# Optimization experiments

Measured on AMD Instinct MI355X. Metric: run time of the kernel, lower is better.

The kernel has to match this reference:

```python
import math
import jax, jax.numpy as jnp
import numpy as np

SCALE = 4; K = 7; R = 3; K2 = K * K
BANDS = 10; FEAT = 64; HID = 256; HEADS = 4
LH = 96; LW = 96; H = LH * SCALE; W = LW * SCALE
IN_DIM = FEAT + 4 * BANDS + 2  # 106
REF_HID = 48  # 3 groups * 16


def _conv(x, w, b, groups=1):
    y = jax.lax.conv_general_dilated(x, w, (1, 1), 'SAME',
        dimension_numbers=('NCHW', 'OIHW', 'NCHW'), feature_group_count=groups)
    return y + b[None, :, None, None]


def _gelu(x):
    return jax.nn.gelu(x, approximate=False)  # torch nn.GELU default (erf)


def _gray(x):  # [B,3,H,W] -> [B,1,H,W]
    return 0.2989 * x[:, 0:1] + 0.587 * x[:, 1:2] + 0.114 * x[:, 2:3]


def setup_inputs() -> dict:
    key = jax.random.key(0)
    ks = iter(jax.random.split(key, 64))
    def W_(sh, s=0.05):
        return (jax.random.normal(next(ks), sh, dtype=jnp.float32) * s)
    def Z_(sh):
        return jnp.zeros(sh, jnp.float32)
    d = {}
    d['lr'] = jax.random.uniform(next(ks), (1, 3, LH, LW), dtype=jnp.float32)
    d['enc_w0'] = W_((FEAT, 3, 3, 3)); d['enc_b0'] = Z_((FEAT,))
    d['enc_w1'] = W_((FEAT, FEAT, 3, 3)); d['enc_b1'] = Z_((FEAT,))
    d['enc_w2'] = W_((FEAT, FEAT, 3, 3)); d['enc_b2'] = Z_((FEAT,))
    d['enc_w3'] = W_((FEAT, FEAT, 3, 3)); d['enc_b3'] = Z_((FEAT,))
    # cond_fuser: 1x1 convs, cond_ch=2 (hover bnd+mask, zeros at inference)
    d['cond_w0'] = W_((FEAT, FEAT + 2, 1, 1)); d['cond_b0'] = Z_((FEAT,))
    d['cond_w1'] = W_((FEAT, FEAT, 1, 1)); d['cond_b1'] = Z_((FEAT,))
    # KernelMLP backbone: 5 Linear layers
    d['mlp_w0'] = W_((IN_DIM, HID)); d['mlp_b0'] = Z_((HID,))
    d['mlp_w1'] = W_((HID, HID)); d['mlp_b1'] = Z_((HID,))
    d['mlp_w2'] = W_((HID, HID)); d['mlp_b2'] = Z_((HID,))
    d['mlp_w3'] = W_((HID, HID)); d['mlp_b3'] = Z_((HID,))
    d['mlp_w4'] = W_((HID, HID)); d['mlp_b4'] = Z_((HID,))
    d['hk_w'] = W_((HID, HEADS * K2)); d['hk_b'] = Z_((HEADS * K2,))
    d['hg_w'] = W_((HID, HEADS)); d['hg_b'] = Z_((HEADS,))
    # ResidualRefiner: grouped convs, groups=3 (OIHW with in/groups channels)
    d['ref_w0'] = W_((REF_HID, 2, 3, 3)); d['ref_b0'] = Z_((REF_HID,))
    d['ref_w1'] = W_((REF_HID, 16, 3, 3)); d['ref_b1'] = Z_((REF_HID,))
    d['ref_w2'] = W_((3, 16, 3, 3)); d['ref_b2'] = Z_((3,))
    return d


def reference(lr, enc_w0, enc_b0, enc_w1, enc_b1, enc_w2, enc_b2, enc_w3, enc_b3,
              cond_w0, cond_b0, cond_w1, cond_b1,
              mlp_w0, mlp_b0, mlp_w1, mlp_b1, mlp_w2, mlp_b2, mlp_w3, mlp_b3,
              mlp_w4, mlp_b4, hk_w, hk_b, hg_w, hg_b,
              ref_w0, ref_b0, ref_w1, ref_b1, ref_w2, ref_b2):
    # --- local CNN features on LR grid ---
    f = _gelu(_conv(lr, enc_w0, enc_b0))
    f = _gelu(_conv(f, enc_w1, enc_b1))
    f = _gelu(_conv(f, enc_w2, enc_b2))
    f = _gelu(_conv(f, enc_w3, enc_b3))
    cond = jnp.zeros((1, 2, LH, LW), f.dtype)  # no hover maps at inference
    f = _conv(jnp.concatenate([f, cond], axis=1), cond_w0, cond_b0)
    f = _conv(_gelu(f), cond_w1, cond_b1)
    # --- bilinear upsample (align_corners=False semantics) ---
    lr_up = jax.image.resize(lr, (1, 3, H, W), method='bilinear')
    # --- HR pixel grid -> LR centers + fractional offsets ---
    yy, xx = jnp.meshgrid(jnp.arange(H), jnp.arange(W), indexing='ij')
    xx = xx.reshape(-1).astype(jnp.float32)
    yy = yy.reshape(-1).astype(jnp.float32)
    lx = (xx + 0.5) / SCALE - 0.5
    ly = (yy + 0.5) / SCALE - 0.5
    cx = jnp.clip(jnp.round(lx), 0, LW - 1)
    cy = jnp.clip(jnp.round(ly), 0, LH - 1)
    dx = (lx - cx)[:, None]
    dy = (ly - cy)[:, None]
    cxi = cx.astype(jnp.int32)
    cyi = cy.astype(jnp.int32)
    idx = cyi * LW + cxi  # flattened gather index [N]
    feat_flat = f[0].reshape(FEAT, -1).T  # [lh*lw, FEAT]
    cf = feat_flat[idx]                   # [N, FEAT]
    # --- Fourier PE of normalized HR coords ---
    xn = (xx + 0.5) / W * 2.0 - 1.0
    yn = (yy + 0.5) / H * 2.0 - 1.0
    freq = (2.0 ** jnp.arange(BANDS, dtype=jnp.float32)) * math.pi
    ax = xn[:, None] * freq[None, :]
    ay = yn[:, None] * freq[None, :]
    pe = jnp.stack([jnp.sin(ax), jnp.cos(ax), jnp.sin(ay), jnp.cos(ay)], axis=-1)
    pe = pe.reshape(-1, 4 * BANDS)  # per-band [sinx,cosx,siny,cosy] order
    # --- per-pixel kernel MLP ---
    z = jnp.concatenate([cf, pe, dx, dy], axis=1)  # [N, 106]
    h = _gelu(z @ mlp_w0 + mlp_b0)
    h = _gelu(h @ mlp_w1 + mlp_b1)
    h = _gelu(h @ mlp_w2 + mlp_b2)
    h = _gelu(h @ mlp_w3 + mlp_b3)
    h = _gelu(h @ mlp_w4 + mlp_b4)
    klog = (h @ hk_w + hk_b).reshape(-1, HEADS, K2)
    glog = h @ hg_w + hg_b
    ker = jax.nn.softmax(klog, axis=-1)   # non-negative kernels
    gate = jax.nn.softmax(glog, axis=-1)  # head mixture
    kmix = jnp.einsum('nh,nhk->nk', gate, ker)  # [N, K2]
    # --- gather KxK LR neighborhood and apply adaptive kernel ---
    oy, ox = jnp.meshgrid(jnp.arange(-R, R + 1), jnp.arange(-R, R + 1), indexing='ij')
    ox = ox.reshape(-1); oy = oy.reshape(-1)  # offsets: oy outer, ox inner
    nx = jnp.clip(cxi[:, None] + ox[None, :], 0, LW - 1)
    ny = jnp.clip(cyi[:, None] + oy[None, :], 0, LH - 1)
    nidx = ny * LW + nx                     # [N, K2]
    lr_flat = lr[0].reshape(3, -1).T        # [lh*lw, 3]
    patches = lr_flat[nidx]                 # [N, K2, 3]
    pred = jnp.einsum('nk,nkc->nc', kmix, patches)  # [N, 3]
    sr = pred.reshape(H, W, 3).transpose(2, 0, 1)[None]  # [1,3,H,W]
    # --- color-safe residual refiner (groups=3) ---
    res0 = sr - lr_up
    x6 = jnp.concatenate([lr_up, res0], axis=1)
    r1 = _gelu(_conv(x6, ref_w0, ref_b0, groups=3))
    r1 = _gelu(_conv(r1, ref_w1, ref_b1, groups=3))
    res = _conv(r1, ref_w2, ref_b2, groups=3)
    sr2 = sr + res
    # --- color-preserving fusion: inject only grayscale residual ---
    delta = _gray(sr2) - _gray(lr_up)
    out = jnp.clip(lr_up + delta, 0.0, 1.0)
    return out
```

## Files before the change

kernel.cpp:

```cpp
#include <hip/hip_runtime.h>
#include <math.h>

#define LWI 96
#define LHI 96
#define HWD 384
#define NPIX 147456
#define LRPIX 9216
#define HID 256

typedef __attribute__((ext_vector_type(8))) _Float16 f16x8;
typedef __attribute__((ext_vector_type(4))) _Float16 f16x4;
typedef __attribute__((ext_vector_type(16))) float f32x16;

__device__ __forceinline__ float gelu_fast(float x){
  float x2 = x*x;
  float u = x*(-2.3021181f - 0.1029443f*x2);
  float e = exp2f(u);
  return x * __builtin_amdgcn_rcpf(1.0f + e);
}

__device__ __forceinline__ float lr_up_at(const float* __restrict__ lr, int c, int y, int x){
  float sy = (y+0.5f)*0.25f - 0.5f;
  float sx = (x+0.5f)*0.25f - 0.5f;
  float fy = floorf(sy), fx = floorf(sx);
  float ty = sy - fy, tx = sx - fx;
  int y0 = (int)fy, x0 = (int)fx;
  int y0c = min(max(y0,0),LHI-1), y1c = min(max(y0+1,0),LHI-1);
  int x0c = min(max(x0,0),LWI-1), x1c = min(max(x0+1,0),LWI-1);
  const float* p = lr + c*LRPIX;
  float v00 = p[y0c*LWI+x0c], v01 = p[y0c*LWI+x1c];
  float v10 = p[y1c*LWI+x0c], v11 = p[y1c*LWI+x1c];
  return (1.f-ty)*((1.f-tx)*v00 + tx*v01) + ty*((1.f-tx)*v10 + tx*v11);
}

__global__ __launch_bounds__(256) void conv3x3_f16out(
    const float* __restrict__ in, const float* __restrict__ w,
    const float* __restrict__ b, _Float16* __restrict__ out16){
  int tid = blockIdx.x*256 + threadIdx.x;
  int o = tid / LRPIX; int rem = tid - o*LRPIX;
  int y = rem / LWI;   int x = rem - y*LWI;
  int ou = __builtin_amdgcn_readfirstlane(o);
  float acc = b[ou];
  const float* wo = w + ou*27;
  for (int i=0;i<3;++i){
    const float* inp = in + i*LRPIX;
    #pragma unroll
    for (int dy=0;dy<3;++dy){
      int yy = y + dy - 1;
      bool yok = (yy>=0 && yy<LHI);
      #pragma unroll
      for (int dx=0;dx<3;++dx){
        int xx = x + dx - 1;
        float v = (yok && xx>=0 && xx<LWI) ? inp[yy*LWI+xx] : 0.0f;
        acc = fmaf(wo[i*9 + dy*3 + dx], v, acc);
      }
    }
  }
  out16[rem*64 + o] = (_Float16)gelu_fast(acc);
}

__global__ __launch_bounds__(256) void pack_convw(
  const float* __restrict__ cw1, const float* __restrict__ cw2,
  const float* __restrict__ cw3, const float* __restrict__ xw0,
  const float* __restrict__ xw1,
  _Float16* __restrict__ WC, _Float16* __restrict__ WX)
{
  int i = blockIdx.x*256 + threadIdx.x;
  if (i < 110592){
    int cv = i / 36864; int s2 = i - cv*36864;
    int tkf = s2 >> 9; int s = s2 & 511;
    int tap = tkf >> 3; int ksfb = tkf & 7;
    int ks = ksfb >> 1; int fb = ksfb & 1;
    int slot = s >> 3; int e = s & 7;
    int oc = fb*32 + (slot & 31);
    int ic = ks*16 + (slot>>5)*8 + e;
    int dy = tap/3, dx = tap - (tap/3)*3;
    const float* src = (cv==0)?cw1:(cv==1)?cw2:cw3;
    WC[i] = (_Float16)src[((oc*64+ic)*3+dy)*3+dx];
  } else if (i < 118784){
    int j = i - 110592;
    int cv = j >> 12; int s2 = j & 4095;
    int ks = s2 >> 10; int fb = (s2 >> 9) & 1; int s = s2 & 511;
    int slot = s >> 3; int e = s & 7;
    int oc = fb*32 + (slot & 31);
    int ic = ks*16 + (slot>>5)*8 + e;
    WX[j] = (_Float16)((cv==0) ? xw0[oc*66+ic] : xw1[oc*64+ic]);
  }
}

__global__ __launch_bounds__(256) void conv_mfma_kernel(
    const _Float16* __restrict__ Xin, const _Float16* __restrict__ WC,
    const float* __restrict__ bias, _Float16* __restrict__ Xout, int cv)
{
  __shared__ _Float16 xs[100*64];
  __shared__ float red[2][2][64][20];
  const int t = threadIdx.x;
  const int lane = t & 63;
  const int w = __builtin_amdgcn_readfirstlane(t >> 6);
  const int fb = w & 1, kh = w >> 1;
  const int g = lane >> 5;
  const int gx0 = blockIdx.x*8, gy0 = blockIdx.y*8;

  for (int i = t; i < 800; i += 256){
    int sp = i >> 3, c = i & 7;
    int ly = (sp*205)>>11; int lx = sp - ly*10;
    int gy = gy0 - 1 + ly, gx = gx0 - 1 + lx;
    f16x8 v = f16x8{};
    if (gy>=0 && gy<LHI && gx>=0 && gx<LWI)
      v = *(const f16x8*)(Xin + (gy*LWI+gx)*64 + c*8);
    *(f16x8*)(xs + sp*64 + ((c ^ (sp&7))*8)) = v;
  }
  __syncthreads();

  const _Float16* WCc = WC + cv*36864;
  const int p0 = lane & 31;
  const int py0 = p0 >> 3, px0 = p0 & 7;
  f32x16 acc0{}, acc1{};
  #pragma unroll
  for (int tap = 0; tap < 9; ++tap){
    const int dy = tap/3, dx = tap - (tap/3)*3;
    #pragma unroll
    for (int ksl = 0; ksl < 2; ++ksl){
      int ks = kh*2 + ksl;
      f16x8 A = *(const f16x8*)(WCc + ((tap*4+ks)*2+fb)*512 + lane*8);
      int sp0 = (py0+dy)*10 + (px0+dx);
      int sp1 = (py0+4+dy)*10 + (px0+dx);
      int c0 = ks*2 + g;
      f16x8 B0 = *(const f16x8*)(xs + sp0*64 + ((c0 ^ (sp0&7))*8));
      f16x8 B1 = *(const f16x8*)(xs + sp1*64 + ((c0 ^ (sp1&7))*8));
      acc0 = __builtin_amdgcn_mfma_f32_32x32x16_f16(A,B0,acc0,0,0,0);
      acc1 = __builtin_amdgcn_mfma_f32_32x32x16_f16(A,B1,acc1,0,0,0);
    }
  }
  if (kh == 1){
    #pragma unroll
    for (int r4=0;r4<4;++r4){
      float4 v0 = make_float4(acc0[r4*4],acc0[r4*4+1],acc0[r4*4+2],acc0[r4*4+3]);
      float4 v1 = make_float4(acc1[r4*4],acc1[r4*4+1],acc1[r4*4+2],acc1[r4*4+3]);
      *(float4*)&red[fb][0][lane][r4*4] = v0;
      *(float4*)&red[fb][1][lane][r4*4] = v1;
    }
  }
  __syncthreads();
  if (kh == 0){
    #pragma unroll
    for (int ph=0; ph<2; ++ph){
      const f32x16& acc = ph ? acc1 : acc0;
      int py = ph*4 + py0;
      int gpx = (gy0+py)*LWI + (gx0+px0);
      #pragma unroll
      for (int r4=0;r4<4;++r4){
        float4 rr = *(const float4*)&red[fb][ph][lane][r4*4];
        float4 bb = *(const float4*)&bias[fb*32 + 8*r4 + 4*g];
        f16x4 o;
        o[0] = (_Float16)gelu_fast(acc[r4*4+0] + rr.x + bb.x);
        o[1] = (_Float16)gelu_fast(acc[r4*4+1] + rr.y + bb.y);
        o[2] = (_Float16)gelu_fast(acc[r4*4+2] + rr.z + bb.z);
        o[3] = (_Float16)gelu_fast(acc[r4*4+3] + rr.w + bb.w);
        *(f16x4*)(Xout + gpx*64 + fb*32 + 8*r4 + 4*g) = o;
      }
    }
  }
}

__global__ __launch_bounds__(256) void conv1x1_mfma(
    const _Float16* __restrict__ Xin, const _Float16* __restrict__ W1,
    const float* __restrict__ bias, _Float16* __restrict__ Xout, int dogelu)
{
  __shared__ _Float16 bufB[4096];
  const int t = threadIdx.x;
  const int lane = t & 63;
  const int w = __builtin_amdgcn_readfirstlane(t >> 6);
  const int fb = w & 1, ph = w >> 1;
  const int px0 = blockIdx.x * 64;
  #pragma unroll
  for (int h = 0; h < 2; ++h){
    int i = t + h*256;
    int p = i & 63, c = i >> 6;
    f16x8 v = *(const f16x8*)(Xin + (px0+p)*64 + c*8);
    *(f16x8*)(bufB + ((c>>1)*2 + (p>>5))*512 + ((p&31)+32*(c&1))*8) = v;
  }
  __syncthreads();
  f32x16 acc{};
  #pragma unroll
  for (int ks=0; ks<4; ++ks){
    f16x8 A = *(const f16x8*)(W1 + (ks*2+fb)*512 + lane*8);
    f16x8 B = *(const f16x8*)(bufB + (ks*2+ph)*512 + lane*8);
    acc = __builtin_amdgcn_mfma_f32_32x32x16_f16(A,B,acc,0,0,0);
  }
  const int p31 = lane & 31, hi = lane >> 5;
  int px = px0 + ph*32 + p31;
  #pragma unroll
  for (int q=0;q<4;++q){
    float4 bb = *(const float4*)&bias[fb*32 + q*8 + 4*hi];
    const float* bp = (const float*)&bb;
    f16x4 o;
    #pragma unroll
    for (int r=0;r<4;++r){
      float v = acc[q*4+r] + bp[r];
      o[r] = (_Float16)(dogelu ? gelu_fast(v) : v);
    }
    *(f16x4*)(Xout + px*64 + fb*32 + q*8 + 4*hi) = o;
  }
}

__global__ __launch_bounds__(256) void pack_weights(
  const float* __restrict__ mw0, const float* __restrict__ mw1,
  const float* __restrict__ mw2, const float* __restrict__ mw3,
  const float* __restrict__ mw4, const float* __restrict__ hkw,
  const float* __restrict__ hgw,
  const float* __restrict__ mb0, const float* __restrict__ mb1,
  const float* __restrict__ mb2, const float* __restrict__ mb3,
  const float* __restrict__ mb4, const float* __restrict__ hkb,
  const float* __restrict__ hgb,
  _Float16* __restrict__ WB, float* __restrict__ biasAll)
{
  int i = blockIdx.x*256 + threadIdx.x;
  if (i < 356352){
    int layer, local;
    if (i < 28672){ layer = 0; local = i; }
    else { layer = 1 + ((i-28672)>>16); local = (i-28672)&65535; }
    int ks = local >> 12; int r = local & 4095;
    int cb = r >> 9; int s2 = r & 511; int slot = s2 >> 3; int e = s2 & 7;
    int col = cb*32 + (slot & 31); int g = slot >> 5;
    int k = ks*16 + g*8 + e;
    float v = 0.f;
    if (layer == 0){ if (k < 106) v = mw0[k*256+col]; }
    else if (layer == 1) v = mw1[k*256+col];
    else if (layer == 2) v = mw2[k*256+col];
    else if (layer == 3) v = mw3[k*256+col];
    else if (layer == 4) v = mw4[k*256+col];
    else { if (col < 196) v = hkw[k*196+col]; else if (col < 200) v = hgw[k*4+col-196]; }
    WB[i] = (_Float16)v;
  } else if (i < 356352+1536){
    int j = i - 356352; int layer = j>>8; int col = j&255;
    float v = 0.f;
    if (layer==0) v=mb0[col]; else if (layer==1) v=mb1[col]; else if(layer==2) v=mb2[col];
    else if(layer==3) v=mb3[col]; else if(layer==4) v=mb4[col];
    else { if (col<196) v=hkb[col]; else if(col<200) v=hgb[col-196]; }
    biasAll[j] = v;
  }
}

template<int NKS>
__device__ __forceinline__ void mlp_pass(const _Float16* __restrict__ Wl,
    const _Float16* __restrict__ buf, int lane, int w, f32x16 (&acc)[2]){
  acc[0] = f32x16{}; acc[1] = f32x16{};
  #pragma unroll
  for (int ks=0; ks<NKS; ++ks){
    f16x8 a = *(const f16x8*)(Wl + (ks*8+w)*512 + lane*8);
    const _Float16* bp = buf + ks*1024 + lane*8;
    f16x8 b0 = *(const f16x8*)(bp);
    f16x8 b1 = *(const f16x8*)(bp + 512);
    acc[0] = __builtin_amdgcn_mfma_f32_32x32x16_f16(a,b0,acc[0],0,0,0);
    acc[1] = __builtin_amdgcn_mfma_f32_32x32x16_f16(a,b1,acc[1],0,0,0);
  }
}

__global__ __launch_bounds__(512,6) void mlp_mfma3_kernel(
  const _Float16* __restrict__ feat16, const float* __restrict__ lr,
  const _Float16* __restrict__ WB, const float* __restrict__ biasAll,
  float* __restrict__ sr)
{
  __shared__ _Float16 buf[16384];
  const int t = threadIdx.x;
  const int lane = t & 63;
  const int w = __builtin_amdgcn_readfirstlane(t >> 6);
  const int p31 = lane & 31; const int hi = lane >> 5;

  {
    const int p = lane; const int q = w;
    const int px = blockIdx.x*64 + p;
    const int y = px / HWD; const int x = px - y*HWD;
    float lx = (x+0.5f)*0.25f - 0.5f;
    float ly = (y+0.5f)*0.25f - 0.5f;
    float cxf = fminf(fmaxf(rintf(lx),0.f),95.f);
    float cyf = fminf(fmaxf(rintf(ly),0.f),95.f);
    int base = (int)cyf*LWI + (int)cxf;
    auto zwrite = [&](int k, float v){
      buf[((k>>4)*2 + (p>>5))*512 + ((p&31) + 32*((k>>3)&1))*8 + (k&7)] = (_Float16)v;
    };
    auto zwriteh = [&](int k, _Float16 v){
      buf[((k>>4)*2 + (p>>5))*512 + ((p&31) + 32*((k>>3)&1))*8 + (k&7)] = v;
    };
    if (q < 2){
      const _Float16* fsrc = feat16 + base*64 + q*32;
      #pragma unroll
      for (int j=0;j<32;++j) zwriteh(q*32+j, fsrc[j]);
    } else if (q == 2){
      float xn = (x+0.5f)/384.0f*2.0f - 1.0f;
      float s = sinf(xn*3.14159265358979323846f);
      float c = cosf(xn*3.14159265358979323846f);
      #pragma unroll
      for (int b=0;b<10;++b){
        zwrite(64+4*b+0, s); zwrite(64+4*b+1, c);
        float s2 = 2.f*s*c; float c2 = 1.f - 2.f*s*s;
        s=s2; c=c2;
      }
      zwrite(104, lx-cxf); zwrite(105, ly-cyf);
    } else if (q == 3){
      float yn = (y+0.5f)/384.0f*2.0f - 1.0f;
      float s = sinf(yn*3.14159265358979323846f);
      float c = cosf(yn*3.14159265358979323846f);
      #pragma unroll
      for (int b=0;b<10;++b){
        zwrite(64+4*b+2, s); zwrite(64+4*b+3, c);
        float s2 = 2.f*s*c; float c2 = 1.f - 2.f*s*s;
        s=s2; c=c2;
      }
    } else if (q == 4){
      #pragma unroll
      for (int k=106;k<112;++k) zwrite(k, 0.f);
    }
  }
  __syncthreads();

  #pragma unroll 1
  for (int L=0; L<5; ++L){
    static const int WOFFS[5] = {0,28672,94208,159744,225280};
    f32x16 acc[2];
    if (L==0) mlp_pass<7>(WB, buf, lane, w, acc);
    else      mlp_pass<16>(WB + WOFFS[L], buf, lane, w, acc);
    __syncthreads();
    const float* Bl = biasAll + L*256;
    #pragma unroll
    for (int q2=0;q2<4;++q2){
      float4 bs = *(const float4*)&Bl[w*32 + q2*8 + 4*hi];
      const float* bp2 = (const float*)&bs;
      int ks2 = w*2 + (q2>>1); int g2 = q2&1;
      _Float16* dst = buf + (ks2*2)*512 + (p31 + 32*g2)*8 + 4*hi;
      #pragma unroll
      for (int pb=0;pb<2;++pb){
        f16x4 o;
        #pragma unroll
        for (int r=0;r<4;++r) o[r] = (_Float16)gelu_fast(acc[pb][q2*4+r] + bp2[r]);
        *(f16x4*)(dst + pb*512) = o;
      }
    }
    __syncthreads();
  }

  {
    f32x16 acc[2];
    if (w < 7) mlp_pass<16>(WB + 290816, buf, lane, w, acc);
    __syncthreads();
    if (w < 7){
      #pragma unroll
      for (int reg=0;reg<16;++reg){
        int f = w*32 + (reg&3) + 8*(reg>>2) + 4*hi;
        if (f < 200){
          float bias = biasAll[1280 + f];
          buf[f*72 + p31]      = (_Float16)(acc[0][reg] + bias);
          buf[f*72 + 32 + p31] = (_Float16)(acc[1][reg] + bias);
        }
      }
    }
  }
  __syncthreads();

  if (t < 256){
    const int p = t & 63; const int hd = t >> 6;
    auto KL = [&](int col)->float { return (float)buf[col*72 + p]; };
    const float L2E = 1.4426950408889634f;
    float g0=KL(196),g1=KL(197),g2=KL(198),g3=KL(199);
    float gm = fmaxf(fmaxf(g0,g1),fmaxf(g2,g3));
    float e0=exp2f((g0-gm)*L2E),e1=exp2f((g1-gm)*L2E),
          e2=exp2f((g2-gm)*L2E),e3=exp2f((g3-gm)*L2E);
    float gate = ((hd==0)?e0:(hd==1)?e1:(hd==2)?e2:e3)/(e0+e1+e2+e3);
    float m = -1e30f;
    #pragma unroll
    for (int k=0;k<49;++k) m = fmaxf(m, KL(hd*49+k));
    float s = 0.f;
    float ev[49];
    #pragma unroll
    for (int k=0;k<49;++k){ float e=exp2f((KL(hd*49+k)-m)*L2E); s+=e; ev[k]=e; }
    float sc = gate/s;
    #pragma unroll
    for (int k=0;k<49;++k) buf[(hd*49+k)*72 + p] = (_Float16)(ev[k]*sc);
  }
  __syncthreads();

  {
    float kv[7];
    #pragma unroll
    for (int j=0;j<7;++j){
      int i = t + j*512;
      if (i < 3136){
        int k = i >> 6, p = i & 63;
        kv[j] = (float)buf[k*72+p] + (float)buf[(49+k)*72+p]
              + (float)buf[(98+k)*72+p] + (float)buf[(147+k)*72+p];
      }
    }
    __syncthreads();
    #pragma unroll
    for (int j=0;j<7;++j){
      int i = t + j*512;
      if (i < 3136){
        int k = i >> 6, p = i & 63;
        buf[k*72+p] = (_Float16)kv[j];
      }
    }
  }
  __syncthreads();

  if (t < 192){
    const int c = t >> 6; const int p = t & 63;
    const int px = blockIdx.x*64 + p;
    const int y = px / HWD; const int x = px - y*HWD;
    float lx = (x+0.5f)*0.25f - 0.5f;
    float ly = (y+0.5f)*0.25f - 0.5f;
    int cxi = (int)fminf(fmaxf(rintf(lx),0.f),95.f);
    int cyi = (int)fminf(fmaxf(rintf(ly),0.f),95.f);
    const float* lrc = lr + c*LRPIX;
    float acc = 0.f;
    bool interior = (cxi>=3 && cxi<=92 && cyi>=3 && cyi<=92);
    if (__all(interior)){
      const float* lrb = lrc + (cyi-3)*LWI + (cxi-3);
      #pragma unroll
      for (int k=0;k<49;++k){
        float km = (float)buf[k*72+p];
        acc = fmaf(km, lrb[(k/7)*LWI + (k - (k/7)*7)], acc);
      }
    } else {
      #pragma unroll
      for (int k=0;k<49;++k){
        float km = (float)buf[k*72+p];
        int oy = k/7 - 3, ox = k - (k/7)*7 - 3;
        int nyy = min(max(cyi+oy,0),95), nxx = min(max(cxi+ox,0),95);
        acc = fmaf(km, lrc[nyy*LWI+nxx], acc);
      }
    }
    sr[c*NPIX + px] = acc;
  }
}

__global__ __launch_bounds__(256) void refiner_group_kernel(
  const float* __restrict__ lr, const float* __restrict__ srg,
  const float* __restrict__ w0, const float* __restrict__ b0,
  const float* __restrict__ w1, const float* __restrict__ b1,
  const float* __restrict__ w2, const float* __restrict__ b2,
  float* __restrict__ resW)
{
  __shared__ float x6s[2][22][26];
  __shared__ float r1a[16][20][20];
  __shared__ float r1b[16][18][20];
  const int g = blockIdx.z;
  const int tid = threadIdx.x;
  const int gx0 = blockIdx.x*16, gy0 = blockIdx.y*16;

  for (int i = tid; i < 2*22*22; i += 256){
    int ic = i / 484; int rem = i - ic*484; int yy = rem / 22; int xx = rem - yy*22;
    int ch = g*2 + ic;
    int gy = gy0 - 3 + yy, gx = gx0 - 3 + xx;
    float v = 0.f;
    if (gy>=0 && gy<HWD && gx>=0 && gx<HWD){
      int c = (ch<3)?ch:(ch-3);
      float lu = lr_up_at(lr, c, gy, gx);
      v = (ch < 3) ? lu : (srg[c*NPIX + gy*HWD + gx] - lu);
    }
    x6s[ic][yy][xx] = v;
  }
  __syncthreads();

  for (int task = tid; task < 320; task += 256){
    int o = task / 20; int yy = task - o*20;
    int og = g*16 + o;
    float bias = b0[og];
    float acc[20];
    #pragma unroll
    for (int j=0;j<20;++j) acc[j] = bias;
    #pragma unroll
    for (int ic=0; ic<2; ++ic){
      #pragma unroll
      for (int dyy=0; dyy<3; ++dyy){
        float row[22];
        #pragma unroll
        for (int j=0;j<22;++j) row[j] = x6s[ic][yy+dyy][j];
        #pragma unroll
        for (int dxx=0; dxx<3; ++dxx){
          float wv = w0[((og*2+ic)*3+dyy)*3+dxx];
          #pragma unroll
          for (int j=0;j<20;++j) acc[j] = fmaf(wv, row[j+dxx], acc[j]);
        }
      }
    }
    int gyy = gy0 - 2 + yy;
    bool rok = (gyy>=0 && gyy<HWD);
    #pragma unroll
    for (int j=0;j<20;++j){
      int gxx = gx0 - 2 + j;
      r1a[o][yy][j] = (rok && gxx>=0 && gxx<HWD) ? gelu_fast(acc[j]) : 0.f;
    }
  }
  __syncthreads();

  for (int task = tid; task < 288; task += 256){
    int o = task / 18; int yy = task - o*18;
    int og = g*16 + o;
    float bias = b1[og];
    float acc[18];
    #pragma unroll
    for (int j=0;j<18;++j) acc[j] = bias;
    for (int ic=0; ic<16; ++ic){
      #pragma unroll
      for (int dyy=0; dyy<3; ++dyy){
        float row[20];
        #pragma unroll
        for (int q=0;q<5;++q)
          *(float4*)&row[q*4] = *(const float4*)&r1a[ic][yy+dyy][q*4];
        #pragma unroll
        for (int dxx=0; dxx<3; ++dxx){
          float wv = w1[((og*16+ic)*3+dyy)*3+dxx];
          #pragma unroll
          for (int j=0;j<18;++j) acc[j] = fmaf(wv, row[j+dxx], acc[j]);
        }
      }
    }
    int gyy = gy0 - 1 + yy;
    bool rok = (gyy>=0 && gyy<HWD);
    #pragma unroll
    for (int j=0;j<18;++j){
      int gxx = gx0 - 1 + j;
      r1b[o][yy][j] = (rok && gxx>=0 && gxx<HWD) ? gelu_fast(acc[j]) : 0.f;
    }
  }
  __syncthreads();

  {
    int ty = tid >> 4, tx = tid & 15;
    float a = b2[g];
    for (int ic=0; ic<16; ++ic){
      #pragma unroll
      for (int dyy=0; dyy<3; ++dyy){
        #pragma unroll
        for (int dxx=0; dxx<3; ++dxx){
          a = fmaf(w2[((g*16+ic)*3+dyy)*3+dxx], r1b[ic][ty+dyy][tx+dxx], a);
        }
      }
    }
    resW[g*NPIX + (gy0+ty)*HWD + gx0+tx] = a;
  }
}

__global__ __launch_bounds__(256) void fuse_kernel(
  const float* __restrict__ lr, const float* __restrict__ srg,
  const float* __restrict__ resW, float* __restrict__ out)
{
  int p = blockIdx.x*256 + threadIdx.x;
  int y = p / HWD, x = p - y*HWD;
  float lu[3];
  float d = 0.f;
  const float cf0=0.2989f, cf1=0.587f, cf2=0.114f;
  lu[0] = lr_up_at(lr, 0, y, x);
  lu[1] = lr_up_at(lr, 1, y, x);
  lu[2] = lr_up_at(lr, 2, y, x);
  d += cf0*(srg[0*NPIX+p] + resW[0*NPIX+p] - lu[0]);
  d += cf1*(srg[1*NPIX+p] + resW[1*NPIX+p] - lu[1]);
  d += cf2*(srg[2*NPIX+p] + resW[2*NPIX+p] - lu[2]);
  #pragma unroll
  for (int c=0;c<3;++c){
    float o_ = lu[c] + d;
    out[c*NPIX + p] = fminf(fmaxf(o_, 0.f), 1.f);
  }
}

extern "C" void kernel_launch(void* const* d_in, const int* in_sizes, int n_in,
                              void* d_out, int out_size, void* d_ws, size_t ws_size,
                              hipStream_t stream){
  const float* lr  = (const float*)d_in[0];
  const float* ew0 = (const float*)d_in[1];  const float* eb0 = (const float*)d_in[2];
  const float* ew1 = (const float*)d_in[3];  const float* eb1 = (const float*)d_in[4];
  const float* ew2 = (const float*)d_in[5];  const float* eb2 = (const float*)d_in[6];
  const float* ew3 = (const float*)d_in[7];  const float* eb3 = (const float*)d_in[8];
  const float* cw0 = (const float*)d_in[9];  const float* cb0 = (const float*)d_in[10];
  const float* cw1 = (const float*)d_in[11]; const float* cb1 = (const float*)d_in[12];
  const float* mw0 = (const float*)d_in[13]; const float* mb0 = (const float*)d_in[14];
  const float* mw1 = (const float*)d_in[15]; const float* mb1 = (const float*)d_in[16];
  const float* mw2 = (const float*)d_in[17]; const float* mb2 = (const float*)d_in[18];
  const float* mw3 = (const float*)d_in[19]; const float* mb3 = (const float*)d_in[20];
  const float* mw4 = (const float*)d_in[21]; const float* mb4 = (const float*)d_in[22];
  const float* hkw = (const float*)d_in[23]; const float* hkb = (const float*)d_in[24];
  const float* hgw = (const float*)d_in[25]; const float* hgb = (const float*)d_in[26];
  const float* rw0 = (const float*)d_in[27]; const float* rb0 = (const float*)d_in[28];
  const float* rw1 = (const float*)d_in[29]; const float* rb1 = (const float*)d_in[30];
  const float* rw2 = (const float*)d_in[31]; const float* rb2 = (const float*)d_in[32];

  float* ws = (float*)d_ws;
  _Float16* X0 = (_Float16*)ws;
  _Float16* X1 = (_Float16*)(ws + 294912);
  float* srp   = ws + 589824;
  _Float16* WB = (_Float16*)(ws + 1032192);
  _Float16* WC = (_Float16*)(ws + 1210368);
  float* biasAll = ws + 1265664;
  float* resW  = ws + 1267200;
  _Float16* WX = (_Float16*)(ws + 1709568);

  pack_weights<<<1398,256,0,stream>>>(mw0,mw1,mw2,mw3,mw4,hkw,hgw,
      mb0,mb1,mb2,mb3,mb4,hkb,hgb, WB, biasAll);
  pack_convw<<<464,256,0,stream>>>(ew1, ew2, ew3, cw0, cw1, WC, WX);

  conv3x3_f16out<<<2304,256,0,stream>>>(lr, ew0, eb0, X0);
  conv_mfma_kernel<<<dim3(12,12),256,0,stream>>>(X0, WC, eb1, X1, 0);
  conv_mfma_kernel<<<dim3(12,12),256,0,stream>>>(X1, WC, eb2, X0, 1);
  conv_mfma_kernel<<<dim3(12,12),256,0,stream>>>(X0, WC, eb3, X1, 2);
  conv1x1_mfma<<<144,256,0,stream>>>(X1, WX,        cb0, X0, 1);
  conv1x1_mfma<<<144,256,0,stream>>>(X0, WX + 4096, cb1, X1, 0);

  mlp_mfma3_kernel<<<2304,512,0,stream>>>(X1, lr, WB, biasAll, srp);

  refiner_group_kernel<<<dim3(24,24,3),256,0,stream>>>(lr, srp,
      rw0,rb0, rw1,rb1, rw2,rb2, resW);
  fuse_kernel<<<576,256,0,stream>>>(lr, srp, resW, (float*)d_out);
}
```

Baseline: 324.0 us.

## Halve conv tile height, double-buffer MLP LDS, widen refiner blocks

The 3x3 MFMA conv now uses 8x4 output tiles with one accumulator per wave, doubling the grid from 144 to 288 blocks so more CUs are busy. The MLP kernel ping-pongs between two LDS buffers, which removes one barrier per layer, and its occupancy hint drops from 6 to 4 to account for the doubled shared memory. The refiner runs with 320 threads so each conv stage finishes in a single pass without a tail loop. The trade-offs are more halo reloads in the conv, lower MLP occupancy, and a partly idle last refiner stage.

```diff
diff --git a/kernel.cpp b/kernel.cpp
--- a/kernel.cpp
+++ b/kernel.cpp
@@ -92,16 +92,16 @@
     const _Float16* __restrict__ Xin, const _Float16* __restrict__ WC,
     const float* __restrict__ bias, _Float16* __restrict__ Xout, int cv)
 {
-  __shared__ _Float16 xs[100*64];
-  __shared__ float red[2][2][64][20];
+  __shared__ _Float16 xs[60*64];
+  __shared__ float red[2][64][20];
   const int t = threadIdx.x;
   const int lane = t & 63;
   const int w = __builtin_amdgcn_readfirstlane(t >> 6);
   const int fb = w & 1, kh = w >> 1;
   const int g = lane >> 5;
-  const int gx0 = blockIdx.x*8, gy0 = blockIdx.y*8;
-
-  for (int i = t; i < 800; i += 256){
+  const int gx0 = blockIdx.x*8, gy0 = blockIdx.y*4;
+
+  for (int i = t; i < 480; i += 256){
     int sp = i >> 3, c = i & 7;
     int ly = (sp*205)>>11; int lx = sp - ly*10;
     int gy = gy0 - 1 + ly, gx = gx0 - 1 + lx;
@@ -115,7 +115,7 @@
   const _Float16* WCc = WC + cv*36864;
   const int p0 = lane & 31;
   const int py0 = p0 >> 3, px0 = p0 & 7;
-  f32x16 acc0{}, acc1{};
+  f32x16 acc0{};
   #pragma unroll
   for (int tap = 0; tap < 9; ++tap){
     const int dy = tap/3, dx = tap - (tap/3)*3;
@@ -124,41 +124,31 @@
       int ks = kh*2 + ksl;
       f16x8 A = *(const f16x8*)(WCc + ((tap*4+ks)*2+fb)*512 + lane*8);
       int sp0 = (py0+dy)*10 + (px0+dx);
-      int sp1 = (py0+4+dy)*10 + (px0+dx);
       int c0 = ks*2 + g;
       f16x8 B0 = *(const f16x8*)(xs + sp0*64 + ((c0 ^ (sp0&7))*8));
-      f16x8 B1 = *(const f16x8*)(xs + sp1*64 + ((c0 ^ (sp1&7))*8));
       acc0 = __builtin_amdgcn_mfma_f32_32x32x16_f16(A,B0,acc0,0,0,0);
-      acc1 = __builtin_amdgcn_mfma_f32_32x32x16_f16(A,B1,acc1,0,0,0);
     }
   }
   if (kh == 1){
     #pragma unroll
     for (int r4=0;r4<4;++r4){
       float4 v0 = make_float4(acc0[r4*4],acc0[r4*4+1],acc0[r4*4+2],acc0[r4*4+3]);
-      float4 v1 = make_float4(acc1[r4*4],acc1[r4*4+1],acc1[r4*4+2],acc1[r4*4+3]);
-      *(float4*)&red[fb][0][lane][r4*4] = v0;
-      *(float4*)&red[fb][1][lane][r4*4] = v1;
+      *(float4*)&red[fb][lane][r4*4] = v0;
     }
   }
   __syncthreads();
   if (kh == 0){
-    #pragma unroll
-    for (int ph=0; ph<2; ++ph){
-      const f32x16& acc = ph ? acc1 : acc0;
-      int py = ph*4 + py0;
-      int gpx = (gy0+py)*LWI + (gx0+px0);
-      #pragma unroll
-      for (int r4=0;r4<4;++r4){
-        float4 rr = *(const float4*)&red[fb][ph][lane][r4*4];
-        float4 bb = *(const float4*)&bias[fb*32 + 8*r4 + 4*g];
-        f16x4 o;
-        o[0] = (_Float16)gelu_fast(acc[r4*4+0] + rr.x + bb.x);
-        o[1] = (_Float16)gelu_fast(acc[r4*4+1] + rr.y + bb.y);
-        o[2] = (_Float16)gelu_fast(acc[r4*4+2] + rr.z + bb.z);
-        o[3] = (_Float16)gelu_fast(acc[r4*4+3] + rr.w + bb.w);
-        *(f16x4*)(Xout + gpx*64 + fb*32 + 8*r4 + 4*g) = o;
-      }
+    int gpx = (gy0+py0)*LWI + (gx0+px0);
+    #pragma unroll
+    for (int r4=0;r4<4;++r4){
+      float4 rr = *(const float4*)&red[fb][lane][r4*4];
+      float4 bb = *(const float4*)&bias[fb*32 + 8*r4 + 4*g];
+      f16x4 o;
+      o[0] = (_Float16)gelu_fast(acc0[r4*4+0] + rr.x + bb.x);
+      o[1] = (_Float16)gelu_fast(acc0[r4*4+1] + rr.y + bb.y);
+      o[2] = (_Float16)gelu_fast(acc0[r4*4+2] + rr.z + bb.z);
+      o[3] = (_Float16)gelu_fast(acc0[r4*4+3] + rr.w + bb.w);
+      *(f16x4*)(Xout + gpx*64 + fb*32 + 8*r4 + 4*g) = o;
     }
   }
 }
@@ -257,12 +247,13 @@
   }
 }
 
-__global__ __launch_bounds__(512,6) void mlp_mfma3_kernel(
+__global__ __launch_bounds__(512,4) void mlp_mfma6_kernel(
   const _Float16* __restrict__ feat16, const float* __restrict__ lr,
   const _Float16* __restrict__ WB, const float* __restrict__ biasAll,
   float* __restrict__ sr)
 {
-  __shared__ _Float16 buf[16384];
+  __shared__ _Float16 bufA[16384];
+  __shared__ _Float16 bufB[16384];
   const int t = threadIdx.x;
   const int lane = t & 63;
   const int w = __builtin_amdgcn_readfirstlane(t >> 6);
@@ -278,10 +269,10 @@
     float cyf = fminf(fmaxf(rintf(ly),0.f),95.f);
     int base = (int)cyf*LWI + (int)cxf;
     auto zwrite = [&](int k, float v){
-      buf[((k>>4)*2 + (p>>5))*512 + ((p&31) + 32*((k>>3)&1))*8 + (k&7)] = (_Float16)v;
+      bufA[((k>>4)*2 + (p>>5))*512 + ((p&31) + 32*((k>>3)&1))*8 + (k&7)] = (_Float16)v;
     };
     auto zwriteh = [&](int k, _Float16 v){
-      buf[((k>>4)*2 + (p>>5))*512 + ((p&31) + 32*((k>>3)&1))*8 + (k&7)] = v;
+      bufA[((k>>4)*2 + (p>>5))*512 + ((p&31) + 32*((k>>3)&1))*8 + (k&7)] = v;
     };
     if (q < 2){
       const _Float16* fsrc = feat16 + base*64 + q*32;
@@ -315,20 +306,22 @@
   }
   __syncthreads();
 
+  _Float16* cur = bufA;
+  _Float16* nxt = bufB;
+
   #pragma unroll 1
   for (int L=0; L<5; ++L){
     static const int WOFFS[5] = {0,28672,94208,159744,225280};
     f32x16 acc[2];
-    if (L==0) mlp_pass<7>(WB, buf, lane, w, acc);
-    else      mlp_pass<16>(WB + WOFFS[L], buf, lane, w, acc);
-    __syncthreads();
+    if (L==0) mlp_pass<7>(WB, cur, lane, w, acc);
+    else      mlp_pass<16>(WB + WOFFS[L], cur, lane, w, acc);
     const float* Bl = biasAll + L*256;
     #pragma unroll
     for (int q2=0;q2<4;++q2){
       float4 bs = *(const float4*)&Bl[w*32 + q2*8 + 4*hi];
       const float* bp2 = (const float*)&bs;
       int ks2 = w*2 + (q2>>1); int g2 = q2&1;
-      _Float16* dst = buf + (ks2*2)*512 + (p31 + 32*g2)*8 + 4*hi;
+      _Float16* dst = nxt + (ks2*2)*512 + (p31 + 32*g2)*8 + 4*hi;
       #pragma unroll
       for (int pb=0;pb<2;++pb){
         f16x4 o;
@@ -338,20 +331,21 @@
       }
     }
     __syncthreads();
-  }
-
+    _Float16* tmp = cur; cur = nxt; nxt = tmp;
+  }
+
+  _Float16* ov = nxt;
   {
     f32x16 acc[2];
-    if (w < 7) mlp_pass<16>(WB + 290816, buf, lane, w, acc);
-    __syncthreads();
     if (w < 7){
+      mlp_pass<16>(WB + 290816, cur, lane, w, acc);
       #pragma unroll
       for (int reg=0;reg<16;++reg){
         int f = w*32 + (reg&3) + 8*(reg>>2) + 4*hi;
         if (f < 200){
           float bias = biasAll[1280 + f];
-          buf[f*72 + p31]      = (_Float16)(acc[0][reg] + bias);
-          buf[f*72 + 32 + p31] = (_Float16)(acc[1][reg] + bias);
+          ov[f*72 + p31]      = (_Float16)(acc[0][reg] + bias);
+          ov[f*72 + 32 + p31] = (_Float16)(acc[1][reg] + bias);
         }
       }
     }
@@ -360,7 +354,7 @@
 
   if (t < 256){
     const int p = t & 63; const int hd = t >> 6;
-    auto KL = [&](int col)->float { return (float)buf[col*72 + p]; };
+    auto KL = [&](int col)->float { return (float)ov[col*72 + p]; };
     const float L2E = 1.4426950408889634f;
     float g0=KL(196),g1=KL(197),g2=KL(198),g3=KL(199);
     float gm = fmaxf(fmaxf(g0,g1),fmaxf(g2,g3));
@@ -376,7 +370,7 @@
     for (int k=0;k<49;++k){ float e=exp2f((KL(hd*49+k)-m)*L2E); s+=e; ev[k]=e; }
     float sc = gate/s;
     #pragma unroll
-    for (int k=0;k<49;++k) buf[(hd*49+k)*72 + p] = (_Float16)(ev[k]*sc);
+    for (int k=0;k<49;++k) ov[(hd*49+k)*72 + p] = (_Float16)(ev[k]*sc);
   }
   __syncthreads();
 
@@ -387,8 +381,8 @@
       int i = t + j*512;
       if (i < 3136){
         int k = i >> 6, p = i & 63;
-        kv[j] = (float)buf[k*72+p] + (float)buf[(49+k)*72+p]
-              + (float)buf[(98+k)*72+p] + (float)buf[(147+k)*72+p];
+        kv[j] = (float)ov[k*72+p] + (float)ov[(49+k)*72+p]
+              + (float)ov[(98+k)*72+p] + (float)ov[(147+k)*72+p];
       }
     }
     __syncthreads();
@@ -397,7 +391,7 @@
       int i = t + j*512;
       if (i < 3136){
         int k = i >> 6, p = i & 63;
-        buf[k*72+p] = (_Float16)kv[j];
+        ov[k*72+p] = (_Float16)kv[j];
       }
     }
   }
@@ -418,13 +412,13 @@
       const float* lrb = lrc + (cyi-3)*LWI + (cxi-3);
       #pragma unroll
       for (int k=0;k<49;++k){
-        float km = (float)buf[k*72+p];
+        float km = (float)ov[k*72+p];
         acc = fmaf(km, lrb[(k/7)*LWI + (k - (k/7)*7)], acc);
       }
     } else {
       #pragma unroll
       for (int k=0;k<49;++k){
-        float km = (float)buf[k*72+p];
+        float km = (float)ov[k*72+p];
         int oy = k/7 - 3, ox = k - (k/7)*7 - 3;
         int nyy = min(max(cyi+oy,0),95), nxx = min(max(cxi+ox,0),95);
         acc = fmaf(km, lrc[nyy*LWI+nxx], acc);
@@ -434,7 +428,7 @@
   }
 }
 
-__global__ __launch_bounds__(256) void refiner_group_kernel(
+__global__ __launch_bounds__(320) void refiner_group_kernel(
   const float* __restrict__ lr, const float* __restrict__ srg,
   const float* __restrict__ w0, const float* __restrict__ b0,
   const float* __restrict__ w1, const float* __restrict__ b1,
@@ -448,7 +442,7 @@
   const int tid = threadIdx.x;
   const int gx0 = blockIdx.x*16, gy0 = blockIdx.y*16;
 
-  for (int i = tid; i < 2*22*22; i += 256){
+  for (int i = tid; i < 2*22*22; i += 320){
     int ic = i / 484; int rem = i - ic*484; int yy = rem / 22; int xx = rem - yy*22;
     int ch = g*2 + ic;
     int gy = gy0 - 3 + yy, gx = gx0 - 3 + xx;
@@ -462,8 +456,8 @@
   }
   __syncthreads();
 
-  for (int task = tid; task < 320; task += 256){
-    int o = task / 20; int yy = task - o*20;
+  if (tid < 320){
+    int o = tid / 20; int yy = tid - o*20;
     int og = g*16 + o;
     float bias = b0[og];
     float acc[20];
@@ -494,8 +488,8 @@
   }
   __syncthreads();
 
-  for (int task = tid; task < 288; task += 256){
-    int o = task / 18; int yy = task - o*18;
+  if (tid < 288){
+    int o = tid / 18; int yy = tid - o*18;
     int og = g*16 + o;
     float bias = b1[og];
     float acc[18];
@@ -526,7 +520,7 @@
   }
   __syncthreads();
 
-  {
+  if (tid < 256){
     int ty = tid >> 4, tx = tid & 15;
     float a = b2[g];
     for (int ic=0; ic<16; ++ic){
@@ -600,15 +594,15 @@
   pack_convw<<<464,256,0,stream>>>(ew1, ew2, ew3, cw0, cw1, WC, WX);
 
   conv3x3_f16out<<<2304,256,0,stream>>>(lr, ew0, eb0, X0);
-  conv_mfma_kernel<<<dim3(12,12),256,0,stream>>>(X0, WC, eb1, X1, 0);
-  conv_mfma_kernel<<<dim3(12,12),256,0,stream>>>(X1, WC, eb2, X0, 1);
-  conv_mfma_kernel<<<dim3(12,12),256,0,stream>>>(X0, WC, eb3, X1, 2);
+  conv_mfma_kernel<<<dim3(12,24),256,0,stream>>>(X0, WC, eb1, X1, 0);
+  conv_mfma_kernel<<<dim3(12,24),256,0,stream>>>(X1, WC, eb2, X0, 1);
+  conv_mfma_kernel<<<dim3(12,24),256,0,stream>>>(X0, WC, eb3, X1, 2);
   conv1x1_mfma<<<144,256,0,stream>>>(X1, WX,        cb0, X0, 1);
   conv1x1_mfma<<<144,256,0,stream>>>(X0, WX + 4096, cb1, X1, 0);
 
-  mlp_mfma3_kernel<<<2304,512,0,stream>>>(X1, lr, WB, biasAll, srp);
-
-  refiner_group_kernel<<<dim3(24,24,3),256,0,stream>>>(lr, srp,
+  mlp_mfma6_kernel<<<2304,512,0,stream>>>(X1, lr, WB, biasAll, srp);
+
+  refiner_group_kernel<<<dim3(24,24,3),320,0,stream>>>(lr, srp,
       rw0,rb0, rw1,rb1, rw2,rb2, resW);
   fuse_kernel<<<576,256,0,stream>>>(lr, srp, resW, (float*)d_out);
 }
```

After: 357.0 us. 10.2% more time.
